# Performance work log

Measured on AMD Instinct MI355X. Metric: run time of the kernel, lower is better.

Reference implementation:

```python
import jax, jax.numpy as jnp
import numpy as np

N, D, C = 8192, 256, 100
MARGIN = 1.0


def setup_inputs() -> dict:
    key = jax.random.key(0)
    k1, k2 = jax.random.split(key)
    features = jax.random.normal(k1, (N, D), dtype=jnp.float32)
    labels = jax.random.randint(k2, (N,), 0, C, dtype=jnp.int64)
    return {"features": features, "labels": labels}


def _pairwise_dist(f):
    # f: [N, D] L2-normalized rows. Euclidean distance matrix [N, N].
    sq = jnp.sum(f * f, axis=1)  # [N]
    d2 = sq[:, None] + sq[None, :] - 2.0 * (f @ f.T)
    d2 = jnp.maximum(d2, 0.0)
    # safe sqrt: zero distance (incl. diagonal) -> 0 with finite grad
    pos = d2 > 0.0
    return jnp.where(pos, jnp.sqrt(jnp.where(pos, d2, 1.0)), 0.0)


def reference(features, labels):
    # F.normalize(p=2, dim=1)
    norm = jnp.linalg.norm(features, axis=1, keepdims=True)
    f = features / jnp.maximum(norm, 1e-12)

    dist = _pairwise_dist(f)  # [N, N]

    onehot = jax.nn.one_hot(labels, C, dtype=f.dtype)  # [N, C]
    counts = jnp.sum(onehot, axis=0)  # [C]
    # S[a, b] = sum_{i in a, j in b} dist[i, j]
    S = onehot.T @ dist @ onehot  # [C, C]

    # intra: per-class mean over off-diagonal pairs (diag of dist is 0),
    # only classes with count > 1, then mean over those classes
    intra_valid = counts > 1.0
    intra_denom = jnp.where(intra_valid, counts * (counts - 1.0), 1.0)
    intra_per_class = jnp.diag(S) / intra_denom
    n_intra = jnp.sum(intra_valid.astype(f.dtype))
    intra = jnp.where(
        n_intra > 0,
        jnp.sum(jnp.where(intra_valid, intra_per_class, 0.0)) / jnp.maximum(n_intra, 1.0),
        0.0,
    )

    # inter: per class-pair (a < b, both present) mean distance, then mean over pairs
    pair_cnt = counts[:, None] * counts[None, :]
    inter_mat = S / jnp.where(pair_cnt > 0.0, pair_cnt, 1.0)
    present = counts > 0.0
    upper = jnp.triu(jnp.ones((C, C), dtype=bool), k=1)
    pair_mask = upper & present[:, None] & present[None, :]
    n_pairs = jnp.sum(pair_mask.astype(f.dtype))
    inter = jnp.where(
        n_pairs > 0,
        jnp.sum(jnp.where(pair_mask, inter_mat, 0.0)) / jnp.maximum(n_pairs, 1.0),
        1.0,
    )

    loss = jax.nn.relu(intra - inter + MARGIN)
    return loss  # scalar; .mean() of a scalar is itself
```

## Files before the change

### kernel.cpp

```cpp
#include <hip/hip_runtime.h>
#include <math.h>

#define N_ROWS 8192
#define D_DIM  256
#define C_CLS  100
#define BM 128
#define BK 32
#define NSTRIP (N_ROWS / BM)
#define NBLK (NSTRIP * (NSTRIP + 1) / 2)
#define UPK (C_CLS * (C_CLS + 1) / 2)
#define NHB (N_ROWS / 256)
#define MAXSEG 4

typedef __attribute__((ext_vector_type(8))) __bf16 bf16x8;
typedef __attribute__((ext_vector_type(4))) float  floatx4;

__device__ __forceinline__ unsigned short f2bf(float x) {
    unsigned int u = __float_as_uint(x);
    u += 0x7fff + ((u >> 16) & 1);
    return (unsigned short)(u >> 16);
}

__device__ __forceinline__ void gl2lds16(const void* g, void* l) {
    __builtin_amdgcn_global_load_lds(
        (const __attribute__((address_space(1))) void*)g,
        (__attribute__((address_space(3))) void*)l, 16, 0, 0);
}

__global__ void hist_k(const int* __restrict__ labels, int* __restrict__ hist_part) {
    __shared__ int h[C_CLS];
    const int t = threadIdx.x;
    if (t < C_CLS) h[t] = 0;
    __syncthreads();
    atomicAdd(&h[labels[blockIdx.x * 256 + t]], 1);
    __syncthreads();
    if (t < C_CLS) hist_part[blockIdx.x * C_CLS + t] = h[t];
}

__global__ void scan_k(const int* __restrict__ hist_part, int* __restrict__ offs,
                       int* __restrict__ blockoffs, float* __restrict__ Ug) {
    __shared__ int tot[C_CLS];
    const int t = threadIdx.x;
    if (t < C_CLS) {
        int run = 0;
        for (int b = 0; b < NHB; ++b) {
            blockoffs[b * C_CLS + t] = run;
            run += hist_part[b * C_CLS + t];
        }
        tot[t] = run;
    }
    __syncthreads();
    if (t == 0) {
        int run = 0;
        for (int c = 0; c < C_CLS; ++c) { offs[c] = run; run += tot[c]; }
        offs[C_CLS] = run;
    }
    for (int e = t; e < UPK; e += 256) Ug[e] = 0.f;
}

__global__ void scatter_k(const int* __restrict__ labels, const int* __restrict__ offs,
                          const int* __restrict__ blockoffs, int* __restrict__ dest,
                          int* __restrict__ slab) {
    __shared__ int cur[C_CLS];
    const int t = threadIdx.x;
    if (t < C_CLS) cur[t] = offs[t] + blockoffs[blockIdx.x * C_CLS + t];
    __syncthreads();
    const int i  = blockIdx.x * 256 + t;
    const int la = labels[i];
    const int pos = atomicAdd(&cur[la], 1);
    dest[i] = pos;
    slab[pos] = la;
}

__global__ void normalize_k(const float* __restrict__ in, const int* __restrict__ dest,
                            unsigned short* __restrict__ fnb) {
    const int row  = blockIdx.x * 4 + (threadIdx.x >> 6);
    const int lane = threadIdx.x & 63;
    float4 v = ((const float4*)in)[row * 64 + lane];
    float s = v.x * v.x + v.y * v.y + v.z * v.z + v.w * v.w;
#pragma unroll
    for (int o = 32; o > 0; o >>= 1) s += __shfl_xor(s, o, 64);
    const float inv = 1.f / fmaxf(sqrtf(s), 1e-12f);
    const int d = dest[row];
    ushort4 o4;
    o4.x = f2bf(v.x * inv); o4.y = f2bf(v.y * inv);
    o4.z = f2bf(v.z * inv); o4.w = f2bf(v.w * inv);
    ((ushort4*)fnb)[d * 64 + lane] = o4;
}

__global__ __launch_bounds__(256, 4)
void main_k(const unsigned short* __restrict__ fnb, const int* __restrict__ slab,
            const int* __restrict__ offs_g, float* __restrict__ Ug) {
    __shared__ __align__(16) unsigned short As[BM * BK];
    __shared__ __align__(16) unsigned short Bs[BM * BK];
    __shared__ float red[4][MAXSEG * MAXSEG][65];
    __shared__ int soffs[C_CLS + 1];
    __shared__ int meta[4][4];

    const int t = threadIdx.x;

    int b = blockIdx.x, ti = 0, len = NSTRIP;
    while (b >= len) { b -= len; ++ti; --len; }
    const int tj = ti + b;
    const int i0 = ti * BM, j0 = tj * BM;

    if (t < C_CLS + 1) soffs[t] = offs_g[t];
    for (int e = t; e < 4 * MAXSEG * MAXSEG * 65; e += 256) (&red[0][0][0])[e] = 0.f;

    const int lane = t & 63;
    const int w    = t >> 6;
    const int m0 = (w & 1) * 64, n0 = (w >> 1) * 64;
    const int lr = lane & 15, lq = lane >> 4;
    const int swz = (lr >> 1) & 3;

    int aoff[4], boff[4];
#pragma unroll
    for (int mb = 0; mb < 4; ++mb) aoff[mb] = (m0 + mb * 16 + lr) * BK + ((lq ^ swz) * 8);
#pragma unroll
    for (int nb = 0; nb < 4; ++nb) boff[nb] = (n0 + nb * 16 + lr) * BK + ((lq ^ swz) * 8);

    const int s0 = t, s1 = t + 256;
    const int r0 = s0 >> 2, kc0 = (s0 & 3) ^ ((r0 >> 1) & 3);
    const int r1 = s1 >> 2, kc1 = (s1 & 3) ^ ((r1 >> 1) & 3);

    floatx4 acc[4][4];
#pragma unroll
    for (int mb = 0; mb < 4; ++mb)
#pragma unroll
        for (int nb = 0; nb < 4; ++nb) acc[mb][nb] = 0.f;

    for (int k0 = 0; k0 < D_DIM; k0 += BK) {
        __syncthreads();
        gl2lds16(&fnb[(size_t)(i0 + r0) * D_DIM + k0 + kc0 * 8], &As[s0 * 8]);
        gl2lds16(&fnb[(size_t)(i0 + r1) * D_DIM + k0 + kc1 * 8], &As[s1 * 8]);
        gl2lds16(&fnb[(size_t)(j0 + r0) * D_DIM + k0 + kc0 * 8], &Bs[s0 * 8]);
        gl2lds16(&fnb[(size_t)(j0 + r1) * D_DIM + k0 + kc1 * 8], &Bs[s1 * 8]);
        __syncthreads();

        bf16x8 a[4], bb[4];
#pragma unroll
        for (int mb = 0; mb < 4; ++mb) a[mb]  = *(const bf16x8*)&As[aoff[mb]];
#pragma unroll
        for (int nb = 0; nb < 4; ++nb) bb[nb] = *(const bf16x8*)&Bs[boff[nb]];
#pragma unroll
        for (int mb = 0; mb < 4; ++mb)
#pragma unroll
            for (int nb = 0; nb < 4; ++nb)
                acc[mb][nb] = __builtin_amdgcn_mfma_f32_16x16x32_bf16(a[mb], bb[nb], acc[mb][nb], 0, 0, 0);
    }

    const bool diag = (ti == tj);
#pragma unroll
    for (int mb = 0; mb < 4; ++mb)
#pragma unroll
        for (int nb = 0; nb < 4; ++nb)
#pragma unroll
            for (int r = 0; r < 4; ++r) {
                const float g = acc[mb][nb][r];
                float dv = __builtin_amdgcn_sqrtf(fmaxf(2.f - 2.f * g, 0.f));
                const int rt = m0 + mb * 16 + lq * 4 + r;
                const int ct = n0 + nb * 16 + lr;
                if (diag && rt == ct) dv = 0.f;
                acc[mb][nb][r] = dv;
            }

    const int cA0 = __builtin_amdgcn_readfirstlane(slab[i0 + m0]);
    const int cA1 = __builtin_amdgcn_readfirstlane(slab[i0 + m0 + 63]);
    const int cB0 = __builtin_amdgcn_readfirstlane(slab[j0 + n0]);
    const int cB1 = __builtin_amdgcn_readfirstlane(slab[j0 + n0 + 63]);
    const int segsA = cA1 - cA0 + 1, segsB = cB1 - cB0 + 1;
    if (lane == 0) { meta[w][0] = cA0; meta[w][1] = cB0; meta[w][2] = segsA; meta[w][3] = segsB; }
    const float wscale = diag ? 1.f : 2.f;

    float rem[4][4];
#pragma unroll
    for (int mb = 0; mb < 4; ++mb)
#pragma unroll
        for (int r = 0; r < 4; ++r)
            rem[mb][r] = acc[mb][0][r] + acc[mb][1][r] + acc[mb][2][r] + acc[mb][3][r];

    for (int sb = 0; sb < segsB; ++sb) {
        const int cb = cB0 + sb;
        float colsum[4][4];
        if (sb == segsB - 1) {
#pragma unroll
            for (int mb = 0; mb < 4; ++mb)
#pragma unroll
                for (int r = 0; r < 4; ++r) colsum[mb][r] = rem[mb][r];
        } else {
            const int rb0 = max(soffs[cb]     - j0, n0);
            const int rb1 = min(soffs[cb + 1] - j0, n0 + 64);
#pragma unroll
            for (int mb = 0; mb < 4; ++mb)
#pragma unroll
                for (int r = 0; r < 4; ++r) colsum[mb][r] = 0.f;
#pragma unroll
            for (int nb = 0; nb < 4; ++nb) {
                const int ct = n0 + nb * 16 + lr;
                const bool ic = (ct >= rb0) & (ct < rb1);
#pragma unroll
                for (int mb = 0; mb < 4; ++mb)
#pragma unroll
                    for (int r = 0; r < 4; ++r)
                        colsum[mb][r] += ic ? acc[mb][nb][r] : 0.f;
            }
#pragma unroll
            for (int mb = 0; mb < 4; ++mb)
#pragma unroll
                for (int r = 0; r < 4; ++r) rem[mb][r] -= colsum[mb][r];
        }
        for (int sa = 0; sa < segsA; ++sa) {
            const int ca = cA0 + sa;
            const int ra0 = max(soffs[ca]     - i0, m0);
            const int ra1 = min(soffs[ca + 1] - i0, m0 + 64);
            float v = 0.f;
#pragma unroll
            for (int mb = 0; mb < 4; ++mb) {
                const int rtb = m0 + mb * 16 + lq * 4;
#pragma unroll
                for (int r = 0; r < 4; ++r) {
                    const int rt = rtb + r;
                    const bool ir = (rt >= ra0) & (rt < ra1);
                    v += ir ? colsum[mb][r] : 0.f;
                }
            }
            if (sa < MAXSEG && sb < MAXSEG) {
                red[w][sb * MAXSEG + sa][lane] = v;
            } else {
#pragma unroll
                for (int o = 32; o > 0; o >>= 1) v += __shfl_xor(v, o, 64);
                if (lane == 0 && v != 0.f) {
                    const int mn = min(ca, cb), mx = max(ca, cb);
                    atomicAdd(&Ug[mx + ((mn * (2 * C_CLS - 1 - mn)) >> 1)], wscale * v);
                }
            }
        }
    }

    __syncthreads();
    {
        const int combo = t >> 2, q = t & 3;
        const int wv = combo >> 4, sl = combo & 15;
        float s = 0.f;
#pragma unroll
        for (int k = 0; k < 16; ++k) s += red[wv][sl][q * 16 + k];
        s += __shfl_xor(s, 1, 64);
        s += __shfl_xor(s, 2, 64);
        const int sa = sl & (MAXSEG - 1), sb = sl >> 2;
        if (q == 0 && sa < meta[wv][2] && sb < meta[wv][3] && s != 0.f) {
            const int ca = meta[wv][0] + sa, cb = meta[wv][1] + sb;
            const int mn = min(ca, cb), mx = max(ca, cb);
            atomicAdd(&Ug[mx + ((mn * (2 * C_CLS - 1 - mn)) >> 1)], wscale * s);
        }
    }
}

__global__ void finalize_k(const float* __restrict__ U, const int* __restrict__ offs,
                           float* __restrict__ out) {
    __shared__ int   cnt[C_CLS];
    __shared__ float rf[256];
    __shared__ int   ri[256];
    const int t = threadIdx.x;
    if (t < C_CLS) cnt[t] = offs[t + 1] - offs[t];
    __syncthreads();

    float s_intra = 0.f; int n_intra = 0;
    if (t < C_CLS) {
        int c = cnt[t];
        if (c > 1) {
            int idx = t + ((t * (2 * C_CLS - 1 - t)) >> 1);
            s_intra = U[idx] / ((float)c * (float)(c - 1));
            n_intra = 1;
        }
    }
    float s_inter = 0.f; int n_pairs = 0;
    for (int p = t; p < C_CLS * C_CLS; p += 256) {
        int a = p / C_CLS, b2 = p - a * C_CLS;
        if (b2 > a && cnt[a] > 0 && cnt[b2] > 0) {
            int idx = b2 + ((a * (2 * C_CLS - 1 - a)) >> 1);
            s_inter += 0.5f * U[idx] / ((float)cnt[a] * (float)cnt[b2]);
            ++n_pairs;
        }
    }

    rf[t] = s_intra; ri[t] = n_intra; __syncthreads();
    for (int s = 128; s > 0; s >>= 1) {
        if (t < s) { rf[t] += rf[t + s]; ri[t] += ri[t + s]; }
        __syncthreads();
    }
    float intra_sum = rf[0]; int intra_n = ri[0];
    __syncthreads();
    rf[t] = s_inter; ri[t] = n_pairs; __syncthreads();
    for (int s = 128; s > 0; s >>= 1) {
        if (t < s) { rf[t] += rf[t + s]; ri[t] += ri[t + s]; }
        __syncthreads();
    }
    if (t == 0) {
        float inter_sum = rf[0]; int pairs_n = ri[0];
        float intra = (intra_n > 0) ? intra_sum / (float)intra_n : 0.f;
        float inter = (pairs_n > 0) ? inter_sum / (float)pairs_n : 1.f;
        out[0] = fmaxf(intra - inter + 1.0f, 0.f);
    }
}

extern "C" void kernel_launch(void* const* d_in, const int* in_sizes, int n_in,
                              void* d_out, int out_size, void* d_ws, size_t ws_size,
                              hipStream_t stream) {
    const float* feats  = (const float*)d_in[0];
    const int*   labels = (const int*)d_in[1];
    float* out = (float*)d_out;

    char* p = (char*)d_ws;
    unsigned short* fnb = (unsigned short*)p;  p += (size_t)N_ROWS * D_DIM * sizeof(unsigned short);
    int*   slab      = (int*)p;  p += (size_t)N_ROWS * sizeof(int);
    int*   dest      = (int*)p;  p += (size_t)N_ROWS * sizeof(int);
    int*   hist_part = (int*)p;  p += (size_t)NHB * C_CLS * sizeof(int);
    int*   blockoffs = (int*)p;  p += (size_t)NHB * C_CLS * sizeof(int);
    int*   offs      = (int*)p;  p += 128 * sizeof(int);
    float* Ug        = (float*)p;

    hist_k    <<<NHB, 256, 0, stream>>>(labels, hist_part);
    scan_k    <<<1, 256, 0, stream>>>(hist_part, offs, blockoffs, Ug);
    scatter_k <<<NHB, 256, 0, stream>>>(labels, offs, blockoffs, dest, slab);
    normalize_k<<<N_ROWS / 4, 256, 0, stream>>>(feats, dest, fnb);
    main_k    <<<NBLK, 256, 0, stream>>>(fnb, slab, offs, Ug);
    finalize_k<<<1, 256, 0, stream>>>(Ug, offs, out);
}
```

Measured before the change: 120.4 us.

## Double K tile, reuse A tile on diagonal blocks, and shrink reduction scratch

```diff
diff --git a/kernel.cpp b/kernel.cpp
--- a/kernel.cpp
+++ b/kernel.cpp
@@ -5,12 +5,12 @@
 #define D_DIM  256
 #define C_CLS  100
 #define BM 128
-#define BK 32
+#define BK 64
 #define NSTRIP (N_ROWS / BM)
 #define NBLK (NSTRIP * (NSTRIP + 1) / 2)
 #define UPK (C_CLS * (C_CLS + 1) / 2)
+#define MAXSEG 4
 #define NHB (N_ROWS / 256)
-#define MAXSEG 4
 
 typedef __attribute__((ext_vector_type(8))) __bf16 bf16x8;
 typedef __attribute__((ext_vector_type(4))) float  floatx4;
@@ -93,7 +93,7 @@
             const int* __restrict__ offs_g, float* __restrict__ Ug) {
     __shared__ __align__(16) unsigned short As[BM * BK];
     __shared__ __align__(16) unsigned short Bs[BM * BK];
-    __shared__ float red[4][MAXSEG * MAXSEG][65];
+    __shared__ float red[4][MAXSEG * MAXSEG][17];
     __shared__ int soffs[C_CLS + 1];
     __shared__ int meta[4][4];
 
@@ -103,25 +103,32 @@
     while (b >= len) { b -= len; ++ti; --len; }
     const int tj = ti + b;
     const int i0 = ti * BM, j0 = tj * BM;
+    const bool diag = (ti == tj);
 
     if (t < C_CLS + 1) soffs[t] = offs_g[t];
-    for (int e = t; e < 4 * MAXSEG * MAXSEG * 65; e += 256) (&red[0][0][0])[e] = 0.f;
 
     const int lane = t & 63;
     const int w    = t >> 6;
     const int m0 = (w & 1) * 64, n0 = (w >> 1) * 64;
     const int lr = lane & 15, lq = lane >> 4;
-    const int swz = (lr >> 1) & 3;
-
-    int aoff[4], boff[4];
-#pragma unroll
-    for (int mb = 0; mb < 4; ++mb) aoff[mb] = (m0 + mb * 16 + lr) * BK + ((lq ^ swz) * 8);
-#pragma unroll
-    for (int nb = 0; nb < 4; ++nb) boff[nb] = (n0 + nb * 16 + lr) * BK + ((lq ^ swz) * 8);
-
-    const int s0 = t, s1 = t + 256;
-    const int r0 = s0 >> 2, kc0 = (s0 & 3) ^ ((r0 >> 1) & 3);
-    const int r1 = s1 >> 2, kc1 = (s1 & 3) ^ ((r1 >> 1) & 3);
+    const int swz = (lr >> 1) & 7;
+
+    int abase[4], bbase[4];
+#pragma unroll
+    for (int mb = 0; mb < 4; ++mb) abase[mb] = (m0 + mb * 16 + lr) * BK;
+#pragma unroll
+    for (int nb = 0; nb < 4; ++nb) bbase[nb] = (n0 + nb * 16 + lr) * BK;
+    const int c0 = (lq ^ swz) * 8;
+    const int c1 = ((lq ^ swz) ^ 4) * 8;
+    const unsigned short* Bsrc = diag ? As : Bs;
+
+    int srow[4], skc[4];
+#pragma unroll
+    for (int u = 0; u < 4; ++u) {
+        const int s = t + 256 * u;
+        srow[u] = s >> 3;
+        skc[u]  = (s & 7) ^ ((srow[u] >> 1) & 7);
+    }
 
     floatx4 acc[4][4];
 #pragma unroll
@@ -129,27 +136,37 @@
 #pragma unroll
         for (int nb = 0; nb < 4; ++nb) acc[mb][nb] = 0.f;
 
+#pragma unroll
     for (int k0 = 0; k0 < D_DIM; k0 += BK) {
         __syncthreads();
-        gl2lds16(&fnb[(size_t)(i0 + r0) * D_DIM + k0 + kc0 * 8], &As[s0 * 8]);
-        gl2lds16(&fnb[(size_t)(i0 + r1) * D_DIM + k0 + kc1 * 8], &As[s1 * 8]);
-        gl2lds16(&fnb[(size_t)(j0 + r0) * D_DIM + k0 + kc0 * 8], &Bs[s0 * 8]);
-        gl2lds16(&fnb[(size_t)(j0 + r1) * D_DIM + k0 + kc1 * 8], &Bs[s1 * 8]);
+#pragma unroll
+        for (int u = 0; u < 4; ++u)
+            gl2lds16(&fnb[(size_t)(i0 + srow[u]) * D_DIM + k0 + skc[u] * 8],
+                     &As[(t + 256 * u) * 8]);
+        if (!diag) {
+#pragma unroll
+            for (int u = 0; u < 4; ++u)
+                gl2lds16(&fnb[(size_t)(j0 + srow[u]) * D_DIM + k0 + skc[u] * 8],
+                         &Bs[(t + 256 * u) * 8]);
+        }
         __syncthreads();
 
-        bf16x8 a[4], bb[4];
-#pragma unroll
-        for (int mb = 0; mb < 4; ++mb) a[mb]  = *(const bf16x8*)&As[aoff[mb]];
-#pragma unroll
-        for (int nb = 0; nb < 4; ++nb) bb[nb] = *(const bf16x8*)&Bs[boff[nb]];
-#pragma unroll
-        for (int mb = 0; mb < 4; ++mb)
-#pragma unroll
-            for (int nb = 0; nb < 4; ++nb)
-                acc[mb][nb] = __builtin_amdgcn_mfma_f32_16x16x32_bf16(a[mb], bb[nb], acc[mb][nb], 0, 0, 0);
-    }
-
-    const bool diag = (ti == tj);
+#pragma unroll
+        for (int h = 0; h < 2; ++h) {
+            const int c = h ? c1 : c0;
+            bf16x8 a[4], bb[4];
+#pragma unroll
+            for (int mb = 0; mb < 4; ++mb) a[mb]  = *(const bf16x8*)&As[abase[mb] + c];
+#pragma unroll
+            for (int nb = 0; nb < 4; ++nb) bb[nb] = *(const bf16x8*)&Bsrc[bbase[nb] + c];
+#pragma unroll
+            for (int mb = 0; mb < 4; ++mb)
+#pragma unroll
+                for (int nb = 0; nb < 4; ++nb)
+                    acc[mb][nb] = __builtin_amdgcn_mfma_f32_16x16x32_bf16(a[mb], bb[nb], acc[mb][nb], 0, 0, 0);
+        }
+    }
+
 #pragma unroll
     for (int mb = 0; mb < 4; ++mb)
 #pragma unroll
@@ -197,12 +214,12 @@
 #pragma unroll
             for (int nb = 0; nb < 4; ++nb) {
                 const int ct = n0 + nb * 16 + lr;
-                const bool ic = (ct >= rb0) & (ct < rb1);
+                const float mk = ((ct >= rb0) & (ct < rb1)) ? 1.f : 0.f;
 #pragma unroll
                 for (int mb = 0; mb < 4; ++mb)
 #pragma unroll
                     for (int r = 0; r < 4; ++r)
-                        colsum[mb][r] += ic ? acc[mb][nb][r] : 0.f;
+                        colsum[mb][r] = fmaf(mk, acc[mb][nb][r], colsum[mb][r]);
             }
 #pragma unroll
             for (int mb = 0; mb < 4; ++mb)
@@ -225,7 +242,9 @@
                 }
             }
             if (sa < MAXSEG && sb < MAXSEG) {
-                red[w][sb * MAXSEG + sa][lane] = v;
+                v += __shfl_xor(v, 1, 64);
+                v += __shfl_xor(v, 2, 64);
+                if ((lane & 3) == 0) red[w][sb * MAXSEG + sa][lane >> 2] = v;
             } else {
 #pragma unroll
                 for (int o = 32; o > 0; o >>= 1) v += __shfl_xor(v, o, 64);
@@ -241,9 +260,8 @@
     {
         const int combo = t >> 2, q = t & 3;
         const int wv = combo >> 4, sl = combo & 15;
-        float s = 0.f;
-#pragma unroll
-        for (int k = 0; k < 16; ++k) s += red[wv][sl][q * 16 + k];
+        float s = red[wv][sl][q * 4 + 0] + red[wv][sl][q * 4 + 1]
+                + red[wv][sl][q * 4 + 2] + red[wv][sl][q * 4 + 3];
         s += __shfl_xor(s, 1, 64);
         s += __shfl_xor(s, 2, 64);
         const int sa = sl & (MAXSEG - 1), sb = sl >> 2;
```

New measurement: 119.5 us. About the same (-0.8%).
